# Kernel optimization log

Hardware: AMD Instinct MI355X
Metric: run time of the kernel (lower is better)

Reference implementation:

```python
import jax, jax.numpy as jnp
import numpy as np

STRIDE, PAD, DIL, DG = 1, 1, 1, 1  # stride, padding, dilation, deformable_groups


def setup_inputs() -> dict:
    key = jax.random.key(0)
    k1, k2, k3, k4 = jax.random.split(key, 4)
    B, C, H, W = 8, 64, 96, 96
    O, K = 64, 3
    x = jax.random.normal(k1, (B, C, H, W), dtype=jnp.float32)
    offset = jax.random.normal(k2, (B, 2 * DG * K * K, H, W), dtype=jnp.float32)
    mask = jax.random.uniform(k3, (B, DG * K * K, H, W), dtype=jnp.float32)
    std = 1.0 / np.sqrt(C * K * K)
    weight = jax.random.uniform(k4, (O, C, K, K), dtype=jnp.float32,
                                minval=-std, maxval=std)
    bias = jnp.zeros((O,), dtype=jnp.float32)
    return {"x": x, "offset": offset, "mask": mask, "weight": weight, "bias": bias}


def _mod_deform_conv(x, offset, mask, weight, bias):
    B, C, H, W = x.shape
    O, _, K, _ = weight.shape
    Ho = (H + 2 * PAD - (DIL * (K - 1) + 1)) // STRIDE + 1
    Wo = (W + 2 * PAD - (DIL * (K - 1) + 1)) // STRIDE + 1
    KK = K * K
    Cg = C // DG

    # base sampling grid: [KK, Ho, Wo]
    py0 = (jnp.arange(Ho) * STRIDE - PAD)[None, None, :, None] + \
          (jnp.arange(K) * DIL)[:, None, None, None]          # [K,1,Ho,1]
    px0 = (jnp.arange(Wo) * STRIDE - PAD)[None, None, None, :] + \
          (jnp.arange(K) * DIL)[None, :, None, None]          # [1,K,1,Wo]
    base_y = jnp.broadcast_to(py0, (K, K, Ho, Wo)).reshape(KK, Ho, Wo)
    base_x = jnp.broadcast_to(px0, (K, K, Ho, Wo)).reshape(KK, Ho, Wo)

    # offsets: channel layout [dg, KK, (y,x)] -> [B, DG, KK, 2, Ho, Wo]
    off = offset.reshape(B, DG, KK, 2, Ho, Wo)
    py = base_y[None, None].astype(x.dtype) + off[:, :, :, 0]  # [B,DG,KK,Ho,Wo]
    px = base_x[None, None].astype(x.dtype) + off[:, :, :, 1]

    y0f = jnp.floor(py); x0f = jnp.floor(px)
    ly = py - y0f; lx = px - x0f
    y0 = y0f.astype(jnp.int32); x0 = x0f.astype(jnp.int32)
    y1 = y0 + 1; x1 = x0 + 1

    x_g = x.reshape(B, DG, Cg, H * W)

    def gather(yi, xi):
        valid = ((yi >= 0) & (yi < H) & (xi >= 0) & (xi < W)).astype(x.dtype)
        idx = jnp.clip(yi, 0, H - 1) * W + jnp.clip(xi, 0, W - 1)  # [B,DG,KK,Ho,Wo]
        flat = jnp.broadcast_to(idx.reshape(B, DG, 1, -1), (B, DG, Cg, KK * Ho * Wo))
        v = jnp.take_along_axis(x_g, flat, axis=-1).reshape(B, DG, Cg, KK, Ho, Wo)
        return v, valid

    v00, m00 = gather(y0, x0)
    v01, m01 = gather(y0, x1)
    v10, m10 = gather(y1, x0)
    v11, m11 = gather(y1, x1)

    w00 = ((1 - ly) * (1 - lx) * m00)[:, :, None]  # [B,DG,1,KK,Ho,Wo]
    w01 = ((1 - ly) * lx * m01)[:, :, None]
    w10 = (ly * (1 - lx) * m10)[:, :, None]
    w11 = (ly * lx * m11)[:, :, None]

    sampled = v00 * w00 + v01 * w01 + v10 * w10 + v11 * w11  # [B,DG,Cg,KK,Ho,Wo]
    # mask modulation
    sampled = sampled * mask.reshape(B, DG, 1, KK, Ho, Wo)

    cols = sampled.reshape(B, C, KK, Ho, Wo)
    out = jnp.einsum('bckhw,ock->bohw', cols, weight.reshape(O, C, KK))
    return out + bias[None, :, None, None]


def reference(x, offset, mask, weight, bias):
    return _mod_deform_conv(x, offset, mask, weight, bias)
```

## Files before the change

kernel.cpp:

```cpp
#include <hip/hip_runtime.h>
#include <hip/hip_bf16.h>


#define B_   8
#define C_   64
#define H_   96
#define W_   96
#define O_   64
#define KK_  9
#define HW_  (H_ * W_)
#define NTILE (HW_ / 64)

typedef __attribute__((ext_vector_type(8))) short short8;
typedef __attribute__((ext_vector_type(4))) float f32x4;
typedef __attribute__((ext_vector_type(4))) unsigned uint4v;

__device__ __forceinline__ unsigned short f2bf(float f) {
    union { float f; unsigned u; } v; v.f = f;
    unsigned r = v.u + 0x7FFF + ((v.u >> 16) & 1);
    return (unsigned short)(r >> 16);
}
__device__ __forceinline__ float bflo(unsigned u) {
    union { unsigned u; float f; } v; v.u = u << 16; return v.f;
}
__device__ __forceinline__ float bfhi(unsigned u) {
    union { unsigned u; float f; } v; v.u = u & 0xffff0000u; return v.f;
}
__device__ __forceinline__ unsigned packbf2(float lo, float hi) {
    __hip_bfloat162 h = __float22bfloat162_rn(make_float2(lo, hi));
    union { __hip_bfloat162 h; unsigned u; } v; v.h = h; return v.u;
}

__global__ __launch_bounds__(256)
void cvt_kernel(const float* __restrict__ x, const float* __restrict__ wgt,
                unsigned short* __restrict__ xT, unsigned short* __restrict__ wsb)
{
    const int t = threadIdx.x;
    if (blockIdx.x < 16) {
        int i = blockIdx.x * 256 + t;
        int o = i >> 6, c = i & 63;
        int ks = c >> 5, hi = (c >> 3) & 3, j = c & 7;
        #pragma unroll
        for (int kk = 0; kk < KK_; ++kk)
            wsb[(size_t)(((kk*2 + ks)*4 + hi)*64 + o)*8 + j] =
                f2bf(wgt[(size_t)(o*64 + c)*KK_ + kk]);
    }
    const int b  = blockIdx.x & 7;
    const int px = (blockIdx.x >> 3) * 256 + t;
    const float* xs = x + (size_t)b * C_ * HW_ + px;
    unsigned pk[32];
    #pragma unroll
    for (int c2 = 0; c2 < 32; ++c2) {
        float lo = xs[(size_t)(2*c2)   * HW_];
        float hi = xs[(size_t)(2*c2+1) * HW_];
        pk[c2] = packbf2(lo, hi);
    }
    uint4v* dst = (uint4v*)(xT + ((size_t)b * HW_ + px) * C_);
    #pragma unroll
    for (int j = 0; j < 8; ++j) {
        uint4v v;
        v.x = pk[4*j]; v.y = pk[4*j+1]; v.z = pk[4*j+2]; v.w = pk[4*j+3];
        dst[j] = v;
    }
}

__global__ __launch_bounds__(256, 2)
void dcn_mfma(const unsigned short* __restrict__ xT,
              const float* __restrict__ offs, const float* __restrict__ mask,
              const unsigned short* __restrict__ wsb,
              const float* __restrict__ bias, float* __restrict__ out)
{
    __shared__ __align__(16) char lds[17536];

    const int t    = threadIdx.x;
    const int lane = t & 63;
    const int wid  = t >> 6;
    const int bi   = blockIdx.x & 7;
    const int tile = blockIdx.x >> 3;
    const int pixbase = tile * 64;

    const int lr = lane & 15, lg = lane >> 4;
    const int px_s = lane >> 2;
    const int q    = lane & 3;

    const int pix = pixbase + wid * 16 + px_s;
    const int ho = pix / W_, wo = pix % W_;
    const float* offp = offs + (size_t)bi * 18 * HW_ + pix;
    const float* mp   = mask + (size_t)bi * 9  * HW_ + pix;
    const unsigned short* xb = xT + (size_t)bi * HW_ * C_ + q * 16;
    char* stg = lds + wid * 4096;

    f32x4 acc[4] = {};

    float coy[2], cox[2], cmv[2];
    uint4v cor[2][8];
    float  cw[2][4];

    coy[0] = offp[0];          cox[0] = offp[HW_];       cmv[0] = mp[0];
    coy[1] = offp[2 * HW_];    cox[1] = offp[3 * HW_];   cmv[1] = mp[HW_];

    auto geom_issue = [&](int k, int s) {
        float py  = (float)(ho - 1 + k / 3) + coy[s];
        float pxf = (float)(wo - 1 + k % 3) + cox[s];
        float y0f = floorf(py), x0f = floorf(pxf);
        float ly = py - y0f, lx = pxf - x0f;
        int y0 = (int)y0f, x0 = (int)x0f;
        int y1 = y0 + 1, x1 = x0 + 1;
        float hy = 1.f - ly, hx = 1.f - lx;
        float mv = cmv[s];
        bool oky0 = (y0 >= 0) & (y0 < H_), oky1 = (y1 >= 0) & (y1 < H_);
        bool okx0 = (x0 >= 0) & (x0 < W_), okx1 = (x1 >= 0) & (x1 < W_);
        cw[s][0] = hy * hx * mv * ((oky0 & okx0) ? 1.f : 0.f);
        cw[s][1] = hy * lx * mv * ((oky0 & okx1) ? 1.f : 0.f);
        cw[s][2] = ly * hx * mv * ((oky1 & okx0) ? 1.f : 0.f);
        cw[s][3] = ly * lx * mv * ((oky1 & okx1) ? 1.f : 0.f);
        int iy0 = min(max(y0, 0), H_ - 1), iy1 = min(max(y1, 0), H_ - 1);
        int ix0 = min(max(x0, 0), W_ - 1), ix1 = min(max(x1, 0), W_ - 1);
        const uint4v* a00 = (const uint4v*)(xb + (size_t)(iy0 * W_ + ix0) * C_);
        const uint4v* a01 = (const uint4v*)(xb + (size_t)(iy0 * W_ + ix1) * C_);
        const uint4v* a10 = (const uint4v*)(xb + (size_t)(iy1 * W_ + ix0) * C_);
        const uint4v* a11 = (const uint4v*)(xb + (size_t)(iy1 * W_ + ix1) * C_);
        cor[s][0] = a00[0]; cor[s][1] = a00[1];
        cor[s][2] = a01[0]; cor[s][3] = a01[1];
        cor[s][4] = a10[0]; cor[s][5] = a10[1];
        cor[s][6] = a11[0]; cor[s][7] = a11[1];
    };

    geom_issue(0, 0);

    #pragma unroll
    for (int kk = 0; kk < KK_; ++kk) {
        const int cur = kk & 1, nxt = cur ^ 1;

        if (kk + 2 < KK_) {
            coy[cur] = offp[(size_t)(2 * kk + 4) * HW_];
            cox[cur] = offp[(size_t)(2 * kk + 5) * HW_];
            cmv[cur] = mp[(size_t)(kk + 2) * HW_];
        }
        if (kk + 1 < KK_) geom_issue(kk + 1, nxt);

        __builtin_amdgcn_sched_barrier(0);

        short8 af[8];
        #pragma unroll
        for (int ks = 0; ks < 2; ++ks)
            #pragma unroll
            for (int m = 0; m < 4; ++m)
                af[ks * 4 + m] = *(const short8*)(wsb +
                    (size_t)((((kk * 2 + ks) * 4 + lg) * 64) + m * 16 + lr) * 8);

        float w00 = cw[cur][0], w01 = cw[cur][1];
        float w10 = cw[cur][2], w11 = cw[cur][3];
        uint4v pkv[2];
        #pragma unroll
        for (int j = 0; j < 8; ++j) {
            unsigned u0 = cor[cur][(j >> 2)][j & 3];
            unsigned u1 = cor[cur][2 + (j >> 2)][j & 3];
            unsigned u2 = cor[cur][4 + (j >> 2)][j & 3];
            unsigned u3 = cor[cur][6 + (j >> 2)][j & 3];
            float lo = fmaf(bflo(u0), w00, fmaf(bflo(u1), w01,
                       fmaf(bflo(u2), w10, bflo(u3) * w11)));
            float hi = fmaf(bfhi(u0), w00, fmaf(bfhi(u1), w01,
                       fmaf(bfhi(u2), w10, bfhi(u3) * w11)));
            if (j < 4) pkv[0][j & 3] = packbf2(lo, hi);
            else       pkv[1][j & 3] = packbf2(lo, hi);
        }
        {
            char* sd = stg + cur * 2048 + px_s * 128;
            int sw = (px_s & 7) << 4;
            *(uint4v*)(sd + ((q * 32) ^ sw))      = pkv[0];
            *(uint4v*)(sd + ((q * 32 + 16) ^ sw)) = pkv[1];
        }
        const char* sbuf = stg + cur * 2048;
        #pragma unroll
        for (int ks = 0; ks < 2; ++ks) {
            int co = ks * 64 + lg * 16;
            short8 bf = *(const short8*)(sbuf + lr * 128 + (co ^ ((lr & 7) << 4)));
            #pragma unroll
            for (int m = 0; m < 4; ++m)
                acc[m] = __builtin_amdgcn_mfma_f32_16x16x32_bf16(
                             af[ks * 4 + m], bf, acc[m], 0, 0, 0);
        }
    }

    __syncthreads();
    float* outb = (float*)lds;
    #pragma unroll
    for (int m = 0; m < 4; ++m)
        #pragma unroll
        for (int r = 0; r < 4; ++r)
            outb[(m * 16 + lg * 4 + r) * 68 + wid * 16 + lr] = acc[m][r];
    __syncthreads();
    #pragma unroll
    for (int r = 0; r < 4; ++r) {
        int idx = t + 256 * r;
        int o = idx >> 4, pq = (idx & 15) * 4;
        float4 v = *(const float4*)&outb[o * 68 + pq];
        float bv = bias[o];
        v.x += bv; v.y += bv; v.z += bv; v.w += bv;
        *(float4*)&out[((size_t)bi * O_ + o) * HW_ + pixbase + pq] = v;
    }
}

extern "C" void kernel_launch(void* const* d_in, const int* in_sizes, int n_in,
                              void* d_out, int out_size, void* d_ws, size_t ws_size,
                              hipStream_t stream)
{
    const float* x    = (const float*)d_in[0];
    const float* offs = (const float*)d_in[1];
    const float* mask = (const float*)d_in[2];
    const float* wgt  = (const float*)d_in[3];
    const float* bias = (const float*)d_in[4];
    float* out = (float*)d_out;

    unsigned short* xT  = (unsigned short*)d_ws;
    unsigned short* wsb = (unsigned short*)((char*)d_ws + 9437184);

    hipLaunchKernelGGL(cvt_kernel, dim3(288), dim3(256), 0, stream,
                       x, wgt, xT, wsb);
    hipLaunchKernelGGL(dcn_mfma, dim3(B_ * NTILE), dim3(256), 0, stream,
                       xT, offs, mask, wsb, bias, out);
}
```

Measured before the change: 43.04 us.

## Compute MFMA B fragments directly in registers, dropping LDS staging

Remaps each lane's work so it gathers and bilinearly blends exactly the channels its MFMA B operand needs: pixel taken from lane&15, channel group from lane>>4, with the two K-halves 32 channels apart. The blended bf16 values go straight into the MFMA without the per-step LDS write and swizzled read. Weight fragment loads are also moved before the sched barrier so they issue earlier. Each pixel's gather is now spread over four lanes with 16-byte loads at two separated offsets instead of 32 contiguous bytes per lane, so memory coalescing changes. The final barrier before the output transpose is removed, which is safe only because LDS is no longer used earlier in the kernel.

After: 65.67 us. 1.53x slower.

```diff
diff --git a/kernel.cpp b/kernel.cpp
--- a/kernel.cpp
+++ b/kernel.cpp
@@ -70,7 +70,7 @@
               const unsigned short* __restrict__ wsb,
               const float* __restrict__ bias, float* __restrict__ out)
 {
-    __shared__ __align__(16) char lds[17536];
+    __shared__ __align__(16) float outb[64 * 68];
 
     const int t    = threadIdx.x;
     const int lane = t & 63;
@@ -80,15 +80,11 @@
     const int pixbase = tile * 64;
 
     const int lr = lane & 15, lg = lane >> 4;
-    const int px_s = lane >> 2;
-    const int q    = lane & 3;
-
-    const int pix = pixbase + wid * 16 + px_s;
+    const int pix = pixbase + wid * 16 + lr;
     const int ho = pix / W_, wo = pix % W_;
     const float* offp = offs + (size_t)bi * 18 * HW_ + pix;
     const float* mp   = mask + (size_t)bi * 9  * HW_ + pix;
-    const unsigned short* xb = xT + (size_t)bi * HW_ * C_ + q * 16;
-    char* stg = lds + wid * 4096;
+    const unsigned short* xb = xT + (size_t)bi * HW_ * C_ + lg * 8;
 
     f32x4 acc[4] = {};
 
@@ -120,10 +116,10 @@
         const uint4v* a01 = (const uint4v*)(xb + (size_t)(iy0 * W_ + ix1) * C_);
         const uint4v* a10 = (const uint4v*)(xb + (size_t)(iy1 * W_ + ix0) * C_);
         const uint4v* a11 = (const uint4v*)(xb + (size_t)(iy1 * W_ + ix1) * C_);
-        cor[s][0] = a00[0]; cor[s][1] = a00[1];
-        cor[s][2] = a01[0]; cor[s][3] = a01[1];
-        cor[s][4] = a10[0]; cor[s][5] = a10[1];
-        cor[s][6] = a11[0]; cor[s][7] = a11[1];
+        cor[s][0] = a00[0]; cor[s][1] = a00[4];
+        cor[s][2] = a01[0]; cor[s][3] = a01[4];
+        cor[s][4] = a10[0]; cor[s][5] = a10[4];
+        cor[s][6] = a11[0]; cor[s][7] = a11[4];
     };
 
     geom_issue(0, 0);
@@ -131,6 +127,14 @@
     #pragma unroll
     for (int kk = 0; kk < KK_; ++kk) {
         const int cur = kk & 1, nxt = cur ^ 1;
+
+        short8 af[8];
+        #pragma unroll
+        for (int ks = 0; ks < 2; ++ks)
+            #pragma unroll
+            for (int m = 0; m < 4; ++m)
+                af[ks * 4 + m] = *(const short8*)(wsb +
+                    (size_t)((((kk * 2 + ks) * 4 + lg) * 64) + m * 16 + lr) * 8);
 
         if (kk + 2 < KK_) {
             coy[cur] = offp[(size_t)(2 * kk + 4) * HW_];
@@ -141,50 +145,34 @@
 
         __builtin_amdgcn_sched_barrier(0);
 
-        short8 af[8];
-        #pragma unroll
-        for (int ks = 0; ks < 2; ++ks)
-            #pragma unroll
-            for (int m = 0; m < 4; ++m)
-                af[ks * 4 + m] = *(const short8*)(wsb +
-                    (size_t)((((kk * 2 + ks) * 4 + lg) * 64) + m * 16 + lr) * 8);
-
         float w00 = cw[cur][0], w01 = cw[cur][1];
         float w10 = cw[cur][2], w11 = cw[cur][3];
-        uint4v pkv[2];
-        #pragma unroll
-        for (int j = 0; j < 8; ++j) {
-            unsigned u0 = cor[cur][(j >> 2)][j & 3];
-            unsigned u1 = cor[cur][2 + (j >> 2)][j & 3];
-            unsigned u2 = cor[cur][4 + (j >> 2)][j & 3];
-            unsigned u3 = cor[cur][6 + (j >> 2)][j & 3];
-            float lo = fmaf(bflo(u0), w00, fmaf(bflo(u1), w01,
-                       fmaf(bflo(u2), w10, bflo(u3) * w11)));
-            float hi = fmaf(bfhi(u0), w00, fmaf(bfhi(u1), w01,
-                       fmaf(bfhi(u2), w10, bfhi(u3) * w11)));
-            if (j < 4) pkv[0][j & 3] = packbf2(lo, hi);
-            else       pkv[1][j & 3] = packbf2(lo, hi);
+        union { uint4v u; short8 s; } b0, b1;
+        #pragma unroll
+        for (int ks = 0; ks < 2; ++ks) {
+            #pragma unroll
+            for (int j = 0; j < 4; ++j) {
+                unsigned u0 = cor[cur][0 + ks][j];
+                unsigned u1 = cor[cur][2 + ks][j];
+                unsigned u2 = cor[cur][4 + ks][j];
+                unsigned u3 = cor[cur][6 + ks][j];
+                float lo = fmaf(bflo(u0), w00, fmaf(bflo(u1), w01,
+                           fmaf(bflo(u2), w10, bflo(u3) * w11)));
+                float hi = fmaf(bfhi(u0), w00, fmaf(bfhi(u1), w01,
+                           fmaf(bfhi(u2), w10, bfhi(u3) * w11)));
+                if (ks == 0) b0.u[j] = packbf2(lo, hi);
+                else         b1.u[j] = packbf2(lo, hi);
+            }
         }
-        {
-            char* sd = stg + cur * 2048 + px_s * 128;
-            int sw = (px_s & 7) << 4;
-            *(uint4v*)(sd + ((q * 32) ^ sw))      = pkv[0];
-            *(uint4v*)(sd + ((q * 32 + 16) ^ sw)) = pkv[1];
-        }
-        const char* sbuf = stg + cur * 2048;
-        #pragma unroll
-        for (int ks = 0; ks < 2; ++ks) {
-            int co = ks * 64 + lg * 16;
-            short8 bf = *(const short8*)(sbuf + lr * 128 + (co ^ ((lr & 7) << 4)));
-            #pragma unroll
-            for (int m = 0; m < 4; ++m)
-                acc[m] = __builtin_amdgcn_mfma_f32_16x16x32_bf16(
-                             af[ks * 4 + m], bf, acc[m], 0, 0, 0);
-        }
-    }
-
-    __syncthreads();
-    float* outb = (float*)lds;
+
+        #pragma unroll
+        for (int m = 0; m < 4; ++m)
+            acc[m] = __builtin_amdgcn_mfma_f32_16x16x32_bf16(af[m],     b0.s, acc[m], 0, 0, 0);
+        #pragma unroll
+        for (int m = 0; m < 4; ++m)
+            acc[m] = __builtin_amdgcn_mfma_f32_16x16x32_bf16(af[4 + m], b1.s, acc[m], 0, 0, 0);
+    }
+
     #pragma unroll
     for (int m = 0; m < 4; ++m)
         #pragma unroll
```
